# Performance work log

Measured on AMD Instinct MI355X. Metric: run time of the kernel, lower is better.

Reference implementation:

```python
import jax, jax.numpy as jnp
import numpy as np

EPS = 1e-5
NEG_SLOPE = 0.2

def _bn(x, gamma, beta):
    # BatchNorm1d in training mode: stats over (batch, length) per channel. x: [B,C,N]
    m = jnp.mean(x, axis=(0, 2), keepdims=True)
    v = jnp.mean((x - m) ** 2, axis=(0, 2), keepdims=True)  # biased variance
    return (x - m) * jax.lax.rsqrt(v + EPS) * gamma[None, :, None] + beta[None, :, None]

def setup_inputs() -> dict:
    key = jax.random.key(0)
    ks = jax.random.split(key, 7)
    B, C, N, H = 32, 64, 2048, 128
    s = 1.0 / np.sqrt(C)
    return {
        "x": jax.random.normal(ks[0], (B, C, N), dtype=jnp.float32),
        "wq": jax.random.normal(ks[1], (C, C), dtype=jnp.float32) * s,
        "wk": jax.random.normal(ks[2], (C, C), dtype=jnp.float32) * s,
        "wv": jax.random.normal(ks[3], (C, C), dtype=jnp.float32) * s,
        "w_ff1": jax.random.normal(ks[4], (H, C), dtype=jnp.float32) * s,
        "w_ff2": jax.random.normal(ks[5], (C, H), dtype=jnp.float32) * (1.0 / np.sqrt(H)),
        "bn1_gamma": jnp.ones((C,), dtype=jnp.float32),
        "bn1_beta": jnp.zeros((C,), dtype=jnp.float32),
        "bn2_gamma": jnp.ones((C,), dtype=jnp.float32),
        "bn2_beta": jnp.zeros((C,), dtype=jnp.float32),
    }

def reference(x, wq, wk, wv, w_ff1, w_ff2, bn1_gamma, bn1_beta, bn2_gamma, bn2_beta):
    # x: [B, C, N]; 1x1 convs are per-point channel matmuls
    C = x.shape[1]
    q = jnp.einsum('oc,bcn->bno', wq, x)          # [B,N,C]
    k = jnp.einsum('oc,bcn->bon', wk, x)          # [B,C,N]
    v = jnp.einsum('oc,bcn->bno', wv, x)          # [B,N,C] (v^T)
    energy = jnp.einsum('bnc,bcm->bnm', q, k)     # [B,N,N]
    attention = jax.nn.softmax(energy / jnp.sqrt(jnp.float32(C)), axis=-1)
    x_r = jnp.einsum('bnm,bmc->bcn', attention, v)  # [B,C,N]
    h = _bn(x + x_r, bn1_gamma, bn1_beta)
    ff = jnp.einsum('hc,bcn->bhn', w_ff1, h)      # [B,H,N]
    ff = jnp.where(ff >= 0, ff, NEG_SLOPE * ff)   # LeakyReLU(0.2)
    ff = jnp.einsum('ch,bhn->bcn', w_ff2, ff)     # [B,C,N]
    return _bn(h + ff, bn2_gamma, bn2_beta)
```

## Files before the change

kernel.cpp:

```cpp
#include <hip/hip_runtime.h>

#define B_ 32
#define C_ 64
#define N_ 2048
#define H_ 128

typedef unsigned short u16;
typedef unsigned int u32;
typedef float f32x4 __attribute__((ext_vector_type(4)));
typedef __bf16 bf16x8 __attribute__((ext_vector_type(8)));
typedef __bf16 bf16x4 __attribute__((ext_vector_type(4)));
typedef unsigned short u16x4 __attribute__((ext_vector_type(4)));

#define MFMA(a, b, c) __builtin_amdgcn_mfma_f32_16x16x32_bf16(a, b, c, 0, 0, 0)
#define LOG2E 1.44269504088896f

__device__ __forceinline__ int swz(int row, int cb) { return row * 128 + (cb ^ ((row & 7) << 4)); }
__device__ __forceinline__ int swz256(int row, int cb) { return row * 256 + (cb ^ ((row & 7) << 4)); }

__device__ __forceinline__ bf16x8 cvt8(const float* p, float s) {
    f32x4 a = *(const f32x4*)p, b = *(const f32x4*)(p + 4);
    bf16x8 o;
    o[0] = (__bf16)(a[0] * s); o[1] = (__bf16)(a[1] * s);
    o[2] = (__bf16)(a[2] * s); o[3] = (__bf16)(a[3] * s);
    o[4] = (__bf16)(b[0] * s); o[5] = (__bf16)(b[1] * s);
    o[6] = (__bf16)(b[2] * s); o[7] = (__bf16)(b[3] * s);
    return o;
}

__global__ __launch_bounds__(256) void qkv_k(
    const float* __restrict__ x,
    const float* __restrict__ wq, const float* __restrict__ wk, const float* __restrict__ wv,
    const float* __restrict__ w1, const float* __restrict__ w2,
    u16* __restrict__ Qg, u16* __restrict__ Kg, u16* __restrict__ Vg,
    u16* __restrict__ w1b, u16* __restrict__ w2b)
{
    const int b = blockIdx.y, nt = blockIdx.x, t = threadIdx.x;
    const int lane = t & 63, wave = t >> 6, g = lane >> 4, r16 = lane & 15;
    __shared__ __align__(16) u16 xT[128 * 64];
    const int n0 = nt * 128;

    bf16x8 wqf[4][2], wkf[4][2], wvf[4][2];
#pragma unroll
    for (int jt = 0; jt < 4; ++jt)
#pragma unroll
        for (int kc = 0; kc < 2; ++kc) {
            const int ro = (r16 + 16 * jt) * 64 + 8 * g + 32 * kc;
            wqf[jt][kc] = cvt8(wq + ro, 0.125f * LOG2E);
            wkf[jt][kc] = cvt8(wk + ro, 1.0f);
            wvf[jt][kc] = cvt8(wv + ro, 1.0f);
        }

    {
        int c = t >> 5;
        const int nn = (t & 31) * 4;
#pragma unroll
        for (int pass = 0; pass < 8; ++pass, c += 8) {
            f32x4 v = *(const f32x4*)&x[(size_t)(b * 64 + c) * 2048 + n0 + nn];
#pragma unroll
            for (int j = 0; j < 4; ++j)
                xT[swz(nn + j, 2 * c) >> 1] = __builtin_bit_cast(u16, (__bf16)v[j]);
        }
    }
    if (b == 0 && nt == 0) {
        for (int i = t; i < H_ * C_; i += 256) w1b[i] = __builtin_bit_cast(u16, (__bf16)w1[i]);
        for (int i = t; i < C_ * H_; i += 256) w2b[i] = __builtin_bit_cast(u16, (__bf16)w2[i]);
    }
    __syncthreads();

#pragma unroll
    for (int p = 0; p < 2; ++p) {
        const int nt16 = wave * 2 + p;
        bf16x8 xa[2];
#pragma unroll
        for (int kc = 0; kc < 2; ++kc)
            xa[kc] = *(const bf16x8*)&xT[swz(nt16 * 16 + r16, 16 * g + 64 * kc) >> 1];
#pragma unroll
        for (int jt = 0; jt < 4; ++jt) {
            f32x4 aq = {0.f, 0.f, 0.f, 0.f}, ak = {0.f, 0.f, 0.f, 0.f};
            aq = MFMA(wqf[jt][0], xa[0], aq); aq = MFMA(wqf[jt][1], xa[1], aq);
            ak = MFMA(wkf[jt][0], xa[0], ak); ak = MFMA(wkf[jt][1], xa[1], ak);
            bf16x4 qk, kk;
#pragma unroll
            for (int r = 0; r < 4; ++r) { qk[r] = (__bf16)aq[r]; kk[r] = (__bf16)ak[r]; }
            const size_t ro = (size_t)(b * 2048 + n0 + nt16 * 16 + r16) * 64 + 16 * jt + 4 * g;
            *(bf16x4*)&Qg[ro] = qk;
            *(bf16x4*)&Kg[ro] = kk;
        }
#pragma unroll
        for (int it = 0; it < 4; ++it) {
            f32x4 av = {0.f, 0.f, 0.f, 0.f};
            av = MFMA(xa[0], wvf[it][0], av);
            av = MFMA(xa[1], wvf[it][1], av);
            bf16x4 vk;
#pragma unroll
            for (int r = 0; r < 4; ++r) vk[r] = (__bf16)av[r];
            *(bf16x4*)&Vg[(size_t)(b * 64 + 16 * it + r16) * 2048 + n0 + nt16 * 16 + 4 * g] = vk;
        }
    }
}

__global__ __launch_bounds__(256) void attn_k(
    const u16* __restrict__ Qg, const u16* __restrict__ Kg, const u16* __restrict__ Vg,
    const float* __restrict__ x, float* __restrict__ y,
    float* __restrict__ ps, float* __restrict__ pq)
{
    const int t = threadIdx.x;
    const int lane = t & 63, wave = t >> 6, g = lane >> 4, r16 = lane & 15;
    const int L = blockIdx.x;
    const int xcd = L & 7, slot = L >> 3;
    const int b = xcd * 4 + (slot >> 4);
    const int qt = slot & 15;

    __shared__ __align__(16) u16 Kt[2][64 * 64];
    __shared__ __align__(16) u16 Vt[2][64 * 64];
    __shared__ __align__(16) u16 Pl[4][2][16 * 64];

    const int n0 = qt * 128 + wave * 32;
    bf16x8 qf[2][2];
#pragma unroll
    for (int u = 0; u < 2; ++u) {
        const u16* qrow = Qg + (size_t)(b * 2048 + n0 + 16 * u + r16) * 64 + 8 * g;
        qf[u][0] = *(const bf16x8*)qrow;
        qf[u][1] = *(const bf16x8*)(qrow + 32);
    }
    f32x4 xr[2][4];
#pragma unroll
    for (int u = 0; u < 2; ++u)
#pragma unroll
        for (int ct = 0; ct < 4; ++ct)
#pragma unroll
            for (int r = 0; r < 4; ++r)
                xr[u][ct][r] = x[(size_t)(b * 64 + 16 * ct + 4 * g + r) * 2048 + n0 + 16 * u + r16];

    f32x4 acc[2][4];
    float m[2] = {-1e30f, -1e30f}, lp[2] = {0.f, 0.f};
#pragma unroll
    for (int u = 0; u < 2; ++u)
#pragma unroll
        for (int ct = 0; ct < 4; ++ct) acc[u][ct] = (f32x4){0.f, 0.f, 0.f, 0.f};

    const char* Kgb = (const char*)Kg + (size_t)b * 2048 * 128;
    const char* Vgb = (const char*)Vg + (size_t)b * 64 * 4096;
    const int srcxor = (((lane & 7) ^ (lane >> 3)) << 4);
    const int rowb = wave * 16 + (lane >> 3);

    auto stage = [&](int kv, int buf) {
#pragma unroll
        for (int j = 0; j < 2; ++j) {
            const char* gk = Kgb + (size_t)(kv + rowb + 8 * j) * 128 + srcxor;
            const char* gv = Vgb + (size_t)(rowb + 8 * j) * 4096 + kv * 2 + srcxor;
            char* lk = (char*)&Kt[buf][0] + (wave * 2 + j) * 1024;
            char* lv = (char*)&Vt[buf][0] + (wave * 2 + j) * 1024;
            __builtin_amdgcn_global_load_lds(
                (const __attribute__((address_space(1))) void*)gk,
                (__attribute__((address_space(3))) void*)lk, 16, 0, 0);
            __builtin_amdgcn_global_load_lds(
                (const __attribute__((address_space(1))) void*)gv,
                (__attribute__((address_space(3))) void*)lv, 16, 0, 0);
        }
    };

    stage(0, 0);

#pragma unroll 1
    for (int kvt = 0; kvt < 32; ++kvt) {
        __syncthreads();
        if (kvt < 31) stage((kvt + 1) * 64, (kvt + 1) & 1);
        const char* Kc = (const char*)&Kt[kvt & 1][0];
        const char* Vc = (const char*)&Vt[kvt & 1][0];

        bf16x8 kf[4][2];
#pragma unroll
        for (int it = 0; it < 4; ++it)
#pragma unroll
            for (int kc = 0; kc < 2; ++kc)
                kf[it][kc] = *(const bf16x8*)(Kc + swz(16 * it + r16, 16 * g + 64 * kc));
        f32x4 s[2][4];
#pragma unroll
        for (int it = 0; it < 4; ++it) {
            f32x4 a0 = {0.f, 0.f, 0.f, 0.f}, a1 = {0.f, 0.f, 0.f, 0.f};
            a0 = MFMA(kf[it][0], qf[0][0], a0); a0 = MFMA(kf[it][1], qf[0][1], a0);
            a1 = MFMA(kf[it][0], qf[1][0], a1); a1 = MFMA(kf[it][1], qf[1][1], a1);
            s[0][it] = a0; s[1][it] = a1;
        }
        bf16x8 vf[4][2];
#pragma unroll
        for (int ct = 0; ct < 4; ++ct)
#pragma unroll
            for (int kc = 0; kc < 2; ++kc)
                vf[ct][kc] = *(const bf16x8*)(Vc + swz(16 * ct + r16, 16 * g + 64 * kc));

#pragma unroll
        for (int u = 0; u < 2; ++u) {
            float pm = s[u][0][0];
#pragma unroll
            for (int it = 0; it < 4; ++it)
#pragma unroll
                for (int r = 0; r < 4; ++r) pm = fmaxf(pm, s[u][it][r]);
            pm = fmaxf(pm, __shfl_xor(pm, 16, 64));
            pm = fmaxf(pm, __shfl_xor(pm, 32, 64));
            if (!__all(pm <= m[u] + 8.f)) {
                const float mn = fmaxf(m[u], pm);
                const float al = exp2f(m[u] - mn);
                m[u] = mn;
                lp[u] *= al;
#pragma unroll
                for (int ct = 0; ct < 4; ++ct)
#pragma unroll
                    for (int r = 0; r < 4; ++r) acc[u][ct][r] *= al;
            }
            float ls = 0.f;
#pragma unroll
            for (int it = 0; it < 4; ++it) {
                bf16x4 pk;
#pragma unroll
                for (int r = 0; r < 4; ++r) {
                    const float pv = exp2f(s[u][it][r] - m[u]);
                    ls += pv;
                    pk[r] = (__bf16)pv;
                }
                *(bf16x4*)((char*)Pl[wave][u] + swz(r16, 32 * it + 8 * g)) = pk;
            }
            lp[u] += ls;
            const bf16x8 pf0 = *(const bf16x8*)((const char*)Pl[wave][u] + swz(r16, 16 * g));
            const bf16x8 pf1 = *(const bf16x8*)((const char*)Pl[wave][u] + swz(r16, 16 * g + 64));
#pragma unroll
            for (int ct = 0; ct < 4; ++ct) {
                acc[u][ct] = MFMA(vf[ct][0], pf0, acc[u][ct]);
                acc[u][ct] = MFMA(vf[ct][1], pf1, acc[u][ct]);
            }
        }
    }

    float sv[4][4], qv[4][4];
#pragma unroll
    for (int ct = 0; ct < 4; ++ct)
#pragma unroll
        for (int r = 0; r < 4; ++r) { sv[ct][r] = 0.f; qv[ct][r] = 0.f; }
#pragma unroll
    for (int u = 0; u < 2; ++u) {
        float l = lp[u];
        l += __shfl_xor(l, 16, 64);
        l += __shfl_xor(l, 32, 64);
        const float inv = 1.0f / l;
        const int n = n0 + 16 * u + r16;
#pragma unroll
        for (int ct = 0; ct < 4; ++ct) {
            f32x4 o;
#pragma unroll
            for (int r = 0; r < 4; ++r) {
                o[r] = acc[u][ct][r] * inv + xr[u][ct][r];
                sv[ct][r] += o[r];
                qv[ct][r] += o[r] * o[r];
            }
            *(f32x4*)&y[(size_t)(b * 2048 + n) * 64 + 16 * ct + 4 * g] = o;
        }
    }
#pragma unroll
    for (int d = 1; d <= 8; d <<= 1)
#pragma unroll
        for (int ct = 0; ct < 4; ++ct)
#pragma unroll
            for (int r = 0; r < 4; ++r) {
                sv[ct][r] += __shfl_xor(sv[ct][r], d, 64);
                qv[ct][r] += __shfl_xor(qv[ct][r], d, 64);
            }
    __syncthreads();
    float* sb = (float*)&Pl[0][0][0];
    if (r16 == 0) {
#pragma unroll
        for (int ct = 0; ct < 4; ++ct)
#pragma unroll
            for (int r = 0; r < 4; ++r) {
                const int c = 16 * ct + 4 * g + r;
                sb[wave * 64 + c] = sv[ct][r];
                sb[256 + wave * 64 + c] = qv[ct][r];
            }
    }
    __syncthreads();
    if (t < 64) {
        ps[L * 64 + t] = sb[t] + sb[64 + t] + sb[128 + t] + sb[192 + t];
        pq[L * 64 + t] = sb[256 + t] + sb[320 + t] + sb[384 + t] + sb[448 + t];
    }
}

__global__ __launch_bounds__(256) void finalize_k(
    const float* __restrict__ psum, const float* __restrict__ psq,
    const float* __restrict__ gamma, const float* __restrict__ beta,
    float* __restrict__ ss, int nblk)
{
    const int c = blockIdx.x, t = threadIdx.x;
    const int lane = t & 63, wave = t >> 6;
    float s = 0.f, q = 0.f;
    for (int bl = t; bl < nblk; bl += 256) {
        s += psum[bl * 64 + c];
        q += psq[bl * 64 + c];
    }
#pragma unroll
    for (int d = 1; d <= 32; d <<= 1) {
        s += __shfl_xor(s, d, 64);
        q += __shfl_xor(q, d, 64);
    }
    __shared__ float ls[4], lq[4];
    if (lane == 0) { ls[wave] = s; lq[wave] = q; }
    __syncthreads();
    if (t == 0) {
        s = ls[0] + ls[1] + ls[2] + ls[3];
        q = lq[0] + lq[1] + lq[2] + lq[3];
        const float mean = s * (1.0f / 65536.0f);
        const float var  = q * (1.0f / 65536.0f) - mean * mean;
        const float sc   = rsqrtf(var + 1e-5f) * gamma[c];
        ss[c] = sc;
        ss[64 + c] = beta[c] - mean * sc;
    }
}

__global__ __launch_bounds__(256) void ff_k(
    const float* __restrict__ y, const float* __restrict__ ss1,
    const u16* __restrict__ w1b, const u16* __restrict__ w2b,
    float* __restrict__ z, float* __restrict__ ps, float* __restrict__ pq)
{
    const int b = blockIdx.y, nt = blockIdx.x, t = threadIdx.x;
    const int lane = t & 63, wave = t >> 6, g = lane >> 4, r16 = lane & 15;
    const int L = blockIdx.y * gridDim.x + blockIdx.x;
    __shared__ __align__(16) u16 hT[64 * 64];
    __shared__ __align__(16) float hf[64 * 68];
    __shared__ __align__(16) u16 pb[4][16 * 128];
    __shared__ float sc1[64], sh1[64];
    if (t < 64) { sc1[t] = ss1[t]; sh1[t] = ss1[64 + t]; }
    __syncthreads();
    const int n0 = nt * 64;
    {
        const int i = t >> 2, c0 = (t & 3) * 16;
        u16 hb[16] __attribute__((aligned(16)));
#pragma unroll
        for (int q4 = 0; q4 < 4; ++q4) {
            const int c = c0 + 4 * q4;
            f32x4 v = *(const f32x4*)&y[(size_t)(b * 2048 + n0 + i) * 64 + c];
            f32x4 hv;
#pragma unroll
            for (int j = 0; j < 4; ++j) hv[j] = v[j] * sc1[c + j] + sh1[c + j];
            *(f32x4*)&hf[i * 68 + c] = hv;
#pragma unroll
            for (int j = 0; j < 4; ++j) hb[4 * q4 + j] = __builtin_bit_cast(u16, (__bf16)hv[j]);
        }
        *(uint4*)&hT[swz(i, 2 * c0) >> 1]      = *(const uint4*)&hb[0];
        *(uint4*)&hT[swz(i, 2 * c0 + 16) >> 1] = *(const uint4*)&hb[8];
    }
    __syncthreads();

    bf16x8 ha[2];
#pragma unroll
    for (int kc = 0; kc < 2; ++kc)
        ha[kc] = *(const bf16x8*)&hT[swz(wave * 16 + r16, 16 * g + 64 * kc) >> 1];
#pragma unroll
    for (int it = 0; it < 8; ++it) {
        f32x4 a = {0.f, 0.f, 0.f, 0.f};
#pragma unroll
        for (int kc = 0; kc < 2; ++kc) {
            bf16x8 w1f = *(const bf16x8*)&w1b[(r16 + 16 * it) * 64 + 8 * g + 32 * kc];
            a = MFMA(w1f, ha[kc], a);
        }
        u16x4 pk;
#pragma unroll
        for (int r = 0; r < 4; ++r) {
            const float rv = a[r] >= 0.f ? a[r] : 0.2f * a[r];
            pk[r] = __builtin_bit_cast(u16, (__bf16)rv);
        }
        *(u16x4*)&pb[wave][swz256(r16, 2 * (16 * it + 4 * g)) >> 1] = pk;
    }
    bf16x8 pa[4];
#pragma unroll
    for (int kc = 0; kc < 4; ++kc)
        pa[kc] = *(const bf16x8*)&pb[wave][swz256(r16, 16 * g + 64 * kc) >> 1];
    const int nl = wave * 16 + r16;
    float sv[4][4], qv[4][4];
#pragma unroll
    for (int jt = 0; jt < 4; ++jt) {
        f32x4 a = {0.f, 0.f, 0.f, 0.f};
#pragma unroll
        for (int kc = 0; kc < 4; ++kc) {
            bf16x8 w2f = *(const bf16x8*)&w2b[(r16 + 16 * jt) * 128 + 8 * g + 32 * kc];
            a = MFMA(w2f, pa[kc], a);
        }
        f32x4 h4 = *(const f32x4*)&hf[nl * 68 + 16 * jt + 4 * g];
#pragma unroll
        for (int r = 0; r < 4; ++r) {
            a[r] += h4[r];
            sv[jt][r] = a[r];
            qv[jt][r] = a[r] * a[r];
        }
        *(f32x4*)&z[(size_t)(b * 2048 + n0 + nl) * 64 + 16 * jt + 4 * g] = a;
    }
#pragma unroll
    for (int d = 1; d <= 8; d <<= 1)
#pragma unroll
        for (int jt = 0; jt < 4; ++jt)
#pragma unroll
            for (int r = 0; r < 4; ++r) {
                sv[jt][r] += __shfl_xor(sv[jt][r], d, 64);
                qv[jt][r] += __shfl_xor(qv[jt][r], d, 64);
            }
    __syncthreads();
    float* sb = (float*)&pb[0][0];
    if (r16 == 0) {
#pragma unroll
        for (int jt = 0; jt < 4; ++jt)
#pragma unroll
            for (int r = 0; r < 4; ++r) {
                const int c = 16 * jt + 4 * g + r;
                sb[wave * 64 + c] = sv[jt][r];
                sb[256 + wave * 64 + c] = qv[jt][r];
            }
    }
    __syncthreads();
    if (t < 64) {
        ps[L * 64 + t] = sb[t] + sb[64 + t] + sb[128 + t] + sb[192 + t];
        pq[L * 64 + t] = sb[256 + t] + sb[320 + t] + sb[384 + t] + sb[448 + t];
    }
}

__global__ __launch_bounds__(256) void bnout_k(
    const float* __restrict__ z, const float* __restrict__ ss2, float* __restrict__ out)
{
    const int b = blockIdx.y, nt = blockIdx.x, t = threadIdx.x;
    __shared__ float tile[64 * 65];
    __shared__ float sc2[64], sh2[64];
    if (t < 64) { sc2[t] = ss2[t]; sh2[t] = ss2[64 + t]; }
    __syncthreads();
    const int n0 = nt * 64;
    {
        const int i = t >> 2, c0 = (t & 3) * 16;
#pragma unroll
        for (int q4 = 0; q4 < 4; ++q4) {
            const int c = c0 + 4 * q4;
            f32x4 v = *(const f32x4*)&z[(size_t)(b * 2048 + n0 + i) * 64 + c];
#pragma unroll
            for (int j = 0; j < 4; ++j)
                tile[(i)*65 + c + j] = v[j] * sc2[c + j] + sh2[c + j];
        }
    }
    __syncthreads();
    {
        const int c = t >> 2, j0 = (t & 3) * 16;
#pragma unroll
        for (int q4 = 0; q4 < 4; ++q4) {
            f32x4 ov;
#pragma unroll
            for (int j = 0; j < 4; ++j)
                ov[j] = tile[(j0 + 4 * q4 + j) * 65 + c];
            *(f32x4*)&out[(size_t)(b * 64 + c) * 2048 + n0 + j0 + 4 * q4] = ov;
        }
    }
}

extern "C" void kernel_launch(void* const* d_in, const int* in_sizes, int n_in,
                              void* d_out, int out_size, void* d_ws, size_t ws_size,
                              hipStream_t stream)
{
    const float* x   = (const float*)d_in[0];
    const float* wq  = (const float*)d_in[1];
    const float* wk  = (const float*)d_in[2];
    const float* wv  = (const float*)d_in[3];
    const float* w1  = (const float*)d_in[4];
    const float* w2  = (const float*)d_in[5];
    const float* g1  = (const float*)d_in[6];
    const float* be1 = (const float*)d_in[7];
    const float* g2  = (const float*)d_in[8];
    const float* be2 = (const float*)d_in[9];
    float* out = (float*)d_out;

    char* w = (char*)d_ws;
    u16* Qg = (u16*)w;   w += (size_t)B_ * N_ * C_ * 2;
    u16* Kg = (u16*)w;   w += (size_t)B_ * N_ * C_ * 2;
    u16* Vg = (u16*)w;   w += (size_t)B_ * N_ * C_ * 2;
    float* y = (float*)w; w += (size_t)B_ * N_ * C_ * 4;
    float* z = (float*)w; w += (size_t)B_ * N_ * C_ * 4;
    u16* w1b = (u16*)w;  w += (size_t)H_ * C_ * 2;
    u16* w2b = (u16*)w;  w += (size_t)C_ * H_ * 2;
    float* ps1 = (float*)w; w += 1024 * 64 * 4;
    float* pq1 = (float*)w; w += 1024 * 64 * 4;
    float* ps2 = (float*)w; w += 1024 * 64 * 4;
    float* pq2 = (float*)w; w += 1024 * 64 * 4;
    float* ss1 = (float*)w; w += 128 * 4;
    float* ss2 = (float*)w; w += 128 * 4;

    const dim3 blk(256);
    hipLaunchKernelGGL(qkv_k,   dim3(16, 32), blk, 0, stream, x, wq, wk, wv, w1, w2, Qg, Kg, Vg, w1b, w2b);
    hipLaunchKernelGGL(attn_k,  dim3(512),    blk, 0, stream, Qg, Kg, Vg, x, y, ps1, pq1);
    hipLaunchKernelGGL(finalize_k, dim3(64),  blk, 0, stream, ps1, pq1, g1, be1, ss1, 512);
    hipLaunchKernelGGL(ff_k,    dim3(32, 32), blk, 0, stream, y, ss1, w1b, w2b, z, ps2, pq2);
    hipLaunchKernelGGL(finalize_k, dim3(64),  blk, 0, stream, ps2, pq2, g2, be2, ss2, 1024);
    hipLaunchKernelGGL(bnout_k, dim3(32, 32), blk, 0, stream, z, ss2, out);
}
```

Baseline: 152.9 us.

## Split attention KV range in two and merge partials in new kernel

The attention kernel now splits the key/value sequence into two halves, doubling the grid to 1024 blocks. Each block writes a bf16 partial output plus a log-sum-exp value. A new merge kernel combines the two partials, adds the residual, writes y and produces the BatchNorm partial statistics. The aim is better occupancy and load balance across CUs, paid for with an extra kernel launch, extra global traffic for the partials, and bf16 rounding of the intermediate outputs.

```diff
diff --git a/kernel.cpp b/kernel.cpp
--- a/kernel.cpp
+++ b/kernel.cpp
@@ -102,19 +102,19 @@
 
 __global__ __launch_bounds__(256) void attn_k(
     const u16* __restrict__ Qg, const u16* __restrict__ Kg, const u16* __restrict__ Vg,
-    const float* __restrict__ x, float* __restrict__ y,
-    float* __restrict__ ps, float* __restrict__ pq)
+    u16* __restrict__ Ob, float* __restrict__ Ml)
 {
     const int t = threadIdx.x;
     const int lane = t & 63, wave = t >> 6, g = lane >> 4, r16 = lane & 15;
     const int L = blockIdx.x;
     const int xcd = L & 7, slot = L >> 3;
-    const int b = xcd * 4 + (slot >> 4);
-    const int qt = slot & 15;
-
-    __shared__ __align__(16) u16 Kt[2][64 * 64];
-    __shared__ __align__(16) u16 Vt[2][64 * 64];
-    __shared__ __align__(16) u16 Pl[4][2][16 * 64];
+    const int b = xcd * 4 + (slot >> 5);
+    const int rem = slot & 31;
+    const int kvh = rem >> 4;
+    const int qt = rem & 15;
+
+    __shared__ __align__(16) u16 Lds16[20480];
+    char* lds = (char*)Lds16;
 
     const int n0 = qt * 128 + wave * 32;
     bf16x8 qf[2][2];
@@ -124,14 +124,6 @@
         qf[u][0] = *(const bf16x8*)qrow;
         qf[u][1] = *(const bf16x8*)(qrow + 32);
     }
-    f32x4 xr[2][4];
-#pragma unroll
-    for (int u = 0; u < 2; ++u)
-#pragma unroll
-        for (int ct = 0; ct < 4; ++ct)
-#pragma unroll
-            for (int r = 0; r < 4; ++r)
-                xr[u][ct][r] = x[(size_t)(b * 64 + 16 * ct + 4 * g + r) * 2048 + n0 + 16 * u + r16];
 
     f32x4 acc[2][4];
     float m[2] = {-1e30f, -1e30f}, lp[2] = {0.f, 0.f};
@@ -140,104 +132,108 @@
 #pragma unroll
         for (int ct = 0; ct < 4; ++ct) acc[u][ct] = (f32x4){0.f, 0.f, 0.f, 0.f};
 
-    const char* Kgb = (const char*)Kg + (size_t)b * 2048 * 128;
-    const char* Vgb = (const char*)Vg + (size_t)b * 64 * 4096;
+    const char* Kgb = (const char*)Kg + ((size_t)b * 2048 + kvh * 1024) * 128;
+    const char* Vgb = (const char*)Vg + (size_t)b * 64 * 4096 + kvh * 2048;
     const int srcxor = (((lane & 7) ^ (lane >> 3)) << 4);
     const int rowb = wave * 16 + (lane >> 3);
 
-    auto stage = [&](int kv, int buf) {
+    int ka[8];
+#pragma unroll
+    for (int i = 0; i < 8; ++i)
+        ka[i] = swz(16 * (i >> 1) + r16, 16 * g + 64 * (i & 1));
+    const int pb0 = 32768 + wave * 2048;
+    int pw[4], pr[2];
+#pragma unroll
+    for (int it = 0; it < 4; ++it) pw[it] = pb0 + swz(r16, 32 * it + 8 * g);
+#pragma unroll
+    for (int kc = 0; kc < 2; ++kc) pr[kc] = pb0 + swz(r16, 16 * g + 64 * kc);
+
+    auto stage = [&](int kvt, int buf) {
 #pragma unroll
         for (int j = 0; j < 2; ++j) {
-            const char* gk = Kgb + (size_t)(kv + rowb + 8 * j) * 128 + srcxor;
-            const char* gv = Vgb + (size_t)(rowb + 8 * j) * 4096 + kv * 2 + srcxor;
-            char* lk = (char*)&Kt[buf][0] + (wave * 2 + j) * 1024;
-            char* lv = (char*)&Vt[buf][0] + (wave * 2 + j) * 1024;
+            const char* gk = Kgb + (size_t)(kvt * 64 + rowb + 8 * j) * 128 + srcxor;
+            const char* gv = Vgb + (size_t)(rowb + 8 * j) * 4096 + kvt * 128 + srcxor;
+            char* lk = lds + buf * 8192 + (wave * 2 + j) * 1024;
             __builtin_amdgcn_global_load_lds(
                 (const __attribute__((address_space(1))) void*)gk,
                 (__attribute__((address_space(3))) void*)lk, 16, 0, 0);
             __builtin_amdgcn_global_load_lds(
                 (const __attribute__((address_space(1))) void*)gv,
-                (__attribute__((address_space(3))) void*)lv, 16, 0, 0);
+                (__attribute__((address_space(3))) void*)(lk + 16384), 16, 0, 0);
         }
     };
 
-    stage(0, 0);
-
-#pragma unroll 1
-    for (int kvt = 0; kvt < 32; ++kvt) {
+    auto tile = [&](int kvt, int buf) {
         __syncthreads();
-        if (kvt < 31) stage((kvt + 1) * 64, (kvt + 1) & 1);
-        const char* Kc = (const char*)&Kt[kvt & 1][0];
-        const char* Vc = (const char*)&Vt[kvt & 1][0];
-
-        bf16x8 kf[4][2];
-#pragma unroll
-        for (int it = 0; it < 4; ++it)
-#pragma unroll
-            for (int kc = 0; kc < 2; ++kc)
-                kf[it][kc] = *(const bf16x8*)(Kc + swz(16 * it + r16, 16 * g + 64 * kc));
+        if (kvt + 1 < 16) stage(kvt + 1, buf ^ 1);
+        const char* Kc = lds + buf * 8192;
+        const char* Vc = Kc + 16384;
+
+        bf16x8 kf[8];
+#pragma unroll
+        for (int i = 0; i < 8; ++i) kf[i] = *(const bf16x8*)(Kc + ka[i]);
         f32x4 s[2][4];
 #pragma unroll
         for (int it = 0; it < 4; ++it) {
             f32x4 a0 = {0.f, 0.f, 0.f, 0.f}, a1 = {0.f, 0.f, 0.f, 0.f};
-            a0 = MFMA(kf[it][0], qf[0][0], a0); a0 = MFMA(kf[it][1], qf[0][1], a0);
-            a1 = MFMA(kf[it][0], qf[1][0], a1); a1 = MFMA(kf[it][1], qf[1][1], a1);
+            a0 = MFMA(kf[2 * it], qf[0][0], a0); a0 = MFMA(kf[2 * it + 1], qf[0][1], a0);
+            a1 = MFMA(kf[2 * it], qf[1][0], a1); a1 = MFMA(kf[2 * it + 1], qf[1][1], a1);
             s[0][it] = a0; s[1][it] = a1;
         }
-        bf16x8 vf[4][2];
-#pragma unroll
-        for (int ct = 0; ct < 4; ++ct)
-#pragma unroll
-            for (int kc = 0; kc < 2; ++kc)
-                vf[ct][kc] = *(const bf16x8*)(Vc + swz(16 * ct + r16, 16 * g + 64 * kc));
+        bf16x8 vf[8];
+#pragma unroll
+        for (int i = 0; i < 8; ++i) vf[i] = *(const bf16x8*)(Vc + ka[i]);
 
 #pragma unroll
         for (int u = 0; u < 2; ++u) {
-            float pm = s[u][0][0];
+            float mi[4];
 #pragma unroll
             for (int it = 0; it < 4; ++it)
-#pragma unroll
-                for (int r = 0; r < 4; ++r) pm = fmaxf(pm, s[u][it][r]);
+                mi[it] = fmaxf(fmaxf(s[u][it][0], s[u][it][1]),
+                               fmaxf(s[u][it][2], s[u][it][3]));
+            float pm = fmaxf(fmaxf(mi[0], mi[1]), fmaxf(mi[2], mi[3]));
             pm = fmaxf(pm, __shfl_xor(pm, 16, 64));
             pm = fmaxf(pm, __shfl_xor(pm, 32, 64));
             if (!__all(pm <= m[u] + 8.f)) {
                 const float mn = fmaxf(m[u], pm);
                 const float al = exp2f(m[u] - mn);
-                m[u] = mn;
-                lp[u] *= al;
+                m[u] = mn; lp[u] *= al;
 #pragma unroll
                 for (int ct = 0; ct < 4; ++ct)
 #pragma unroll
                     for (int r = 0; r < 4; ++r) acc[u][ct][r] *= al;
             }
-            float ls = 0.f;
+            float ts[4];
 #pragma unroll
             for (int it = 0; it < 4; ++it) {
+                const float p0 = exp2f(s[u][it][0] - m[u]);
+                const float p1 = exp2f(s[u][it][1] - m[u]);
+                const float p2 = exp2f(s[u][it][2] - m[u]);
+                const float p3 = exp2f(s[u][it][3] - m[u]);
+                ts[it] = (p0 + p1) + (p2 + p3);
                 bf16x4 pk;
-#pragma unroll
-                for (int r = 0; r < 4; ++r) {
-                    const float pv = exp2f(s[u][it][r] - m[u]);
-                    ls += pv;
-                    pk[r] = (__bf16)pv;
-                }
-                *(bf16x4*)((char*)Pl[wave][u] + swz(r16, 32 * it + 8 * g)) = pk;
+                pk[0] = (__bf16)p0; pk[1] = (__bf16)p1;
+                pk[2] = (__bf16)p2; pk[3] = (__bf16)p3;
+                *(bf16x4*)(lds + pw[it]) = pk;
             }
-            lp[u] += ls;
-            const bf16x8 pf0 = *(const bf16x8*)((const char*)Pl[wave][u] + swz(r16, 16 * g));
-            const bf16x8 pf1 = *(const bf16x8*)((const char*)Pl[wave][u] + swz(r16, 16 * g + 64));
+            lp[u] += (ts[0] + ts[1]) + (ts[2] + ts[3]);
+            const bf16x8 pf0 = *(const bf16x8*)(lds + pr[0]);
+            const bf16x8 pf1 = *(const bf16x8*)(lds + pr[1]);
 #pragma unroll
             for (int ct = 0; ct < 4; ++ct) {
-                acc[u][ct] = MFMA(vf[ct][0], pf0, acc[u][ct]);
-                acc[u][ct] = MFMA(vf[ct][1], pf1, acc[u][ct]);
+                acc[u][ct] = MFMA(vf[2 * ct], pf0, acc[u][ct]);
+                acc[u][ct] = MFMA(vf[2 * ct + 1], pf1, acc[u][ct]);
             }
         }
-    }
-
-    float sv[4][4], qv[4][4];
-#pragma unroll
-    for (int ct = 0; ct < 4; ++ct)
-#pragma unroll
-        for (int r = 0; r < 4; ++r) { sv[ct][r] = 0.f; qv[ct][r] = 0.f; }
+    };
+
+    stage(0, 0);
+#pragma unroll 1
+    for (int kvt = 0; kvt < 16; kvt += 2) {
+        tile(kvt, 0);
+        tile(kvt + 1, 1);
+    }
+
 #pragma unroll
     for (int u = 0; u < 2; ++u) {
         float l = lp[u];
@@ -245,43 +241,61 @@
         l += __shfl_xor(l, 32, 64);
         const float inv = 1.0f / l;
         const int n = n0 + 16 * u + r16;
+        const size_t ob = ((size_t)(kvh * 32 + b) * 2048 + n) * 64;
 #pragma unroll
         for (int ct = 0; ct < 4; ++ct) {
-            f32x4 o;
-#pragma unroll
-            for (int r = 0; r < 4; ++r) {
-                o[r] = acc[u][ct][r] * inv + xr[u][ct][r];
-                sv[ct][r] += o[r];
-                qv[ct][r] += o[r] * o[r];
-            }
-            *(f32x4*)&y[(size_t)(b * 2048 + n) * 64 + 16 * ct + 4 * g] = o;
-        }
-    }
-#pragma unroll
-    for (int d = 1; d <= 8; d <<= 1)
-#pragma unroll
-        for (int ct = 0; ct < 4; ++ct)
-#pragma unroll
-            for (int r = 0; r < 4; ++r) {
-                sv[ct][r] += __shfl_xor(sv[ct][r], d, 64);
-                qv[ct][r] += __shfl_xor(qv[ct][r], d, 64);
-            }
-    __syncthreads();
-    float* sb = (float*)&Pl[0][0][0];
-    if (r16 == 0) {
-#pragma unroll
-        for (int ct = 0; ct < 4; ++ct)
-#pragma unroll
-            for (int r = 0; r < 4; ++r) {
-                const int c = 16 * ct + 4 * g + r;
-                sb[wave * 64 + c] = sv[ct][r];
-                sb[256 + wave * 64 + c] = qv[ct][r];
-            }
-    }
+            bf16x4 ov;
+#pragma unroll
+            for (int r = 0; r < 4; ++r) ov[r] = (__bf16)(acc[u][ct][r] * inv);
+            *(bf16x4*)&Ob[ob + 16 * ct + 4 * g] = ov;
+        }
+        if (lane < 16)
+            Ml[(size_t)(kvh * 32 + b) * 2048 + n0 + 16 * u + lane] = m[u] + log2f(l);
+    }
+}
+
+__global__ __launch_bounds__(256) void merge_k(
+    const u16* __restrict__ Ob, const float* __restrict__ Ml,
+    const float* __restrict__ x, float* __restrict__ y,
+    float* __restrict__ ps, float* __restrict__ pq)
+{
+    const int b = blockIdx.y, nt = blockIdx.x, t = threadIdx.x;
+    const int n0 = nt * 64;
+    __shared__ float xT[64 * 65];
+    __shared__ float sred[8][64];
+    {
+        const int c = t >> 2, nn = (t & 3) * 16;
+#pragma unroll
+        for (int q4 = 0; q4 < 4; ++q4) {
+            f32x4 v = *(const f32x4*)&x[(size_t)(b * 64 + c) * 2048 + n0 + nn + 4 * q4];
+#pragma unroll
+            for (int j = 0; j < 4; ++j) xT[(nn + 4 * q4 + j) * 65 + c] = v[j];
+        }
+    }
+    __syncthreads();
+    const int c = t & 63, rg = t >> 6;
+    float s = 0.f, q = 0.f;
+    const __bf16* O0 = (const __bf16*)Ob + ((size_t)b * 2048 + n0) * 64;
+    const __bf16* O1 = (const __bf16*)Ob + ((size_t)(32 + b) * 2048 + n0) * 64;
+    const float* Ml0 = Ml + (size_t)b * 2048 + n0;
+    const float* Ml1 = Ml + (size_t)(32 + b) * 2048 + n0;
+#pragma unroll 4
+    for (int i = rg; i < 64; i += 4) {
+        const float w0l = Ml0[i], w1l = Ml1[i];
+        const float M = fmaxf(w0l, w1l);
+        const float w0 = exp2f(w0l - M), w1 = exp2f(w1l - M);
+        const float inv = 1.0f / (w0 + w1);
+        const float o0 = (float)O0[i * 64 + c], o1 = (float)O1[i * 64 + c];
+        const float val = (w0 * o0 + w1 * o1) * inv + xT[i * 65 + c];
+        y[((size_t)b * 2048 + n0 + i) * 64 + c] = val;
+        s += val; q += val * val;
+    }
+    sred[rg][c] = s; sred[4 + rg][c] = q;
     __syncthreads();
     if (t < 64) {
-        ps[L * 64 + t] = sb[t] + sb[64 + t] + sb[128 + t] + sb[192 + t];
-        pq[L * 64 + t] = sb[256 + t] + sb[320 + t] + sb[384 + t] + sb[448 + t];
+        const int LL = b * 32 + nt;
+        ps[LL * 64 + t] = sred[0][t] + sred[1][t] + sred[2][t] + sred[3][t];
+        pq[LL * 64 + t] = sred[4][t] + sred[5][t] + sred[6][t] + sred[7][t];
     }
 }
 
@@ -477,8 +491,10 @@
     u16* Vg = (u16*)w;   w += (size_t)B_ * N_ * C_ * 2;
     float* y = (float*)w; w += (size_t)B_ * N_ * C_ * 4;
     float* z = (float*)w; w += (size_t)B_ * N_ * C_ * 4;
+    u16* Ob = (u16*)z;
     u16* w1b = (u16*)w;  w += (size_t)H_ * C_ * 2;
     u16* w2b = (u16*)w;  w += (size_t)C_ * H_ * 2;
+    float* Ml  = (float*)w; w += (size_t)2 * B_ * N_ * 4;
     float* ps1 = (float*)w; w += 1024 * 64 * 4;
     float* pq1 = (float*)w; w += 1024 * 64 * 4;
     float* ps2 = (float*)w; w += 1024 * 64 * 4;
@@ -488,8 +504,9 @@
 
     const dim3 blk(256);
     hipLaunchKernelGGL(qkv_k,   dim3(16, 32), blk, 0, stream, x, wq, wk, wv, w1, w2, Qg, Kg, Vg, w1b, w2b);
-    hipLaunchKernelGGL(attn_k,  dim3(512),    blk, 0, stream, Qg, Kg, Vg, x, y, ps1, pq1);
-    hipLaunchKernelGGL(finalize_k, dim3(64),  blk, 0, stream, ps1, pq1, g1, be1, ss1, 512);
+    hipLaunchKernelGGL(attn_k,  dim3(1024),   blk, 0, stream, Qg, Kg, Vg, Ob, Ml);
+    hipLaunchKernelGGL(merge_k, dim3(32, 32), blk, 0, stream, Ob, Ml, x, y, ps1, pq1);
+    hipLaunchKernelGGL(finalize_k, dim3(64),  blk, 0, stream, ps1, pq1, g1, be1, ss1, 1024);
     hipLaunchKernelGGL(ff_k,    dim3(32, 32), blk, 0, stream, y, ss1, w1b, w2b, z, ps2, pq2);
     hipLaunchKernelGGL(finalize_k, dim3(64),  blk, 0, stream, ps2, pq2, g2, be2, ss2, 1024);
     hipLaunchKernelGGL(bnout_k, dim3(32, 32), blk, 0, stream, z, ss2, out);
```

New measurement: 157.4 us. 2.9% more time.
